# Kernel optimization log

Hardware: AMD Instinct MI355X
Metric: run time of the kernel (lower is better)

The kernel has to match this reference:

```python
import jax, jax.numpy as jnp
import numpy as np

PATCH_SIZES = (16, 32, 48, 64)
RES_IDX = (0, 1, 2, 3)  # min(int(s*4/3), 3) for s in 0..3
QUANT_RESI = 0.5
BETA = 0.25
D = 32      # embedding_dim == input channels
V = 2048    # vocab_size
G = 8       # GroupNorm groups
EPS = 1e-5


def conv3(x, w, b):
    y = jax.lax.conv_general_dilated(x, w, (1, 1), 'SAME', dimension_numbers=('NCHW', 'OIHW', 'NCHW'))
    return y + b[None, :, None, None]


def group_norm(x, gamma, beta):
    n, c, h, w = x.shape
    xr = x.reshape(n, G, c // G, h, w)
    mu = xr.mean(axis=(2, 3, 4), keepdims=True)
    var = xr.var(axis=(2, 3, 4), keepdims=True)
    xn = ((xr - mu) * jax.lax.rsqrt(var + EPS)).reshape(n, c, h, w)
    return xn * gamma[None, :, None, None] + beta[None, :, None, None]


def conv_block(x, w1, b1, gamma, beta, w2, b2):
    h = conv3(x, w1, b1)
    h = jax.nn.gelu(group_norm(h, gamma, beta), approximate=False)
    return conv3(h, w2, b2)


def _forward(x, emb, pw1, pb1, pg, pbt, pw2, pb2, rw1, rb1, rg, rbt, rw2, rb2):
    B, C, H, W = x.shape
    acc = jnp.zeros_like(x)
    total_loss = jnp.zeros((), x.dtype)
    idx_list = []
    for s, p in enumerate(PATCH_SIZES):
        nh, nw = H // p, W // p
        # unfold: non-overlapping patches -> (B*N, C, p, p), N row-major over (nh, nw)
        patches = (x - acc).reshape(B, C, nh, p, nw, p).transpose(0, 2, 4, 1, 3, 5).reshape(B * nh * nw, C, p, p)
        z = conv_block(patches, pw1[s], pb1[s], pg[s], pbt[s], pw2[s], pb2[s])
        zf = z.reshape(-1, D)  # raw row-major reshape, exactly as the torch code does
        d = (zf * zf).sum(1, keepdims=True) + (emb * emb).sum(1) - 2.0 * (zf @ emb.T)
        idx = jnp.argmin(d, axis=1)
        zq = emb[idx].reshape(z.shape)
        loss = jnp.mean((jax.lax.stop_gradient(zq) - z) ** 2) + BETA * jnp.mean((zq - jax.lax.stop_gradient(z)) ** 2)
        total_loss = total_loss + loss
        zq = z + jax.lax.stop_gradient(zq - z)  # straight-through estimator
        r = RES_IDX[s]
        zq = zq * (1.0 - QUANT_RESI) + conv_block(zq, rw1[r], rb1[r], rg[r], rbt[r], rw2[r], rb2[r]) * QUANT_RESI
        # fold: exact inverse of unfold (patch sizes divide H, W)
        decoded = zq.reshape(B, nh, nw, C, p, p).transpose(0, 3, 1, 4, 2, 5).reshape(B, C, H, W)
        acc = acc + decoded
        idx_list.append(idx.reshape(B, -1))
    return (jax.nn.sigmoid(acc), *idx_list, total_loss)


def setup_inputs() -> dict:
    key = jax.random.key(0)
    ks = jax.random.split(key, 4)
    S = len(PATCH_SIZES)
    x = jax.random.normal(ks[0], (1, D, 384, 384), dtype=jnp.float32)
    emb = jax.random.uniform(ks[1], (V, D), jnp.float32, -1.0 / V, 1.0 / V)

    def wset(k):
        k1, k2, k3, k4 = jax.random.split(k, 4)
        return (jax.random.normal(k1, (S, D, D, 3, 3), jnp.float32) * 0.05,
                jax.random.normal(k2, (S, D), jnp.float32) * 0.02,
                jnp.ones((S, D), jnp.float32),
                jnp.zeros((S, D), jnp.float32),
                jax.random.normal(k3, (S, D, D, 3, 3), jnp.float32) * 0.05,
                jax.random.normal(k4, (S, D), jnp.float32) * 0.02)

    pw1, pb1, pg, pbt, pw2, pb2 = wset(ks[2])
    rw1, rb1, rg, rbt, rw2, rb2 = wset(ks[3])
    return {"x": x, "emb": emb,
            "pw1": pw1, "pb1": pb1, "pg": pg, "pbt": pbt, "pw2": pw2, "pb2": pb2,
            "rw1": rw1, "rb1": rb1, "rg": rg, "rbt": rbt, "rw2": rw2, "rb2": rb2}


def reference(x, emb, pw1, pb1, pg, pbt, pw2, pb2, rw1, rb1, rg, rbt, rw2, rb2):
    return _forward(x, emb, pw1, pb1, pg, pbt, pw2, pb2, rw1, rb1, rg, rbt, rw2, rb2)
```

## Files before the change

kernel.cpp:

```cpp
#include <hip/hip_runtime.h>
#include <cmath>

#define WIDTH 384
#define HW 147456
#define CHW 4718592
#define NCH 32
#define NV 2048
#define NROWS 147456

typedef short vshort8 __attribute__((ext_vector_type(8)));
typedef float vfloat4 __attribute__((ext_vector_type(4)));

__device__ inline unsigned short bf_split(float x, float& back) {
  unsigned int b; __builtin_memcpy(&b, &x, 4);
  unsigned int r = (b + 0x7FFFu + ((b >> 16) & 1u)) >> 16;
  unsigned int bb = r << 16; float f; __builtin_memcpy(&f, &bb, 4);
  back = f; return (unsigned short)r;
}

template <int SQ>
__device__ float np_pw(const float* a, int n, float mu) {
  if (n < 8) {
    float res = 0.0f;
    for (int i = 0; i < n; i++) {
      float v = a[i];
      if (SQ) { float d = __fsub_rn(v, mu); v = __fmul_rn(d, d); }
      res = __fadd_rn(res, v);
    }
    return res;
  }
  if (n <= 128) {
    float r[8];
#pragma unroll
    for (int j = 0; j < 8; j++) {
      float v = a[j];
      if (SQ) { float d = __fsub_rn(v, mu); v = __fmul_rn(d, d); }
      r[j] = v;
    }
    int i;
    for (i = 8; i + 8 <= n; i += 8) {
#pragma unroll
      for (int j = 0; j < 8; j++) {
        float v = a[i + j];
        if (SQ) { float d = __fsub_rn(v, mu); v = __fmul_rn(d, d); }
        r[j] = __fadd_rn(r[j], v);
      }
    }
    float res = __fadd_rn(__fadd_rn(__fadd_rn(r[0], r[1]), __fadd_rn(r[2], r[3])),
                          __fadd_rn(__fadd_rn(r[4], r[5]), __fadd_rn(r[6], r[7])));
    for (; i < n; i++) {
      float v = a[i];
      if (SQ) { float d = __fsub_rn(v, mu); v = __fmul_rn(d, d); }
      res = __fadd_rn(res, v);
    }
    return res;
  }
  int n2 = n / 2; n2 -= n2 % 8;
  return __fadd_rn(np_pw<SQ>(a, n2, mu), np_pw<SQ>(a + n2, n - n2, mu));
}

__global__ __launch_bounds__(256) void prep_kernel(
    const float* __restrict__ pw1, const float* __restrict__ pw2,
    const float* __restrict__ rw1, const float* __restrict__ rw2,
    const float* __restrict__ emb, float* __restrict__ wt, float* __restrict__ ee,
    unsigned short* __restrict__ eh, unsigned short* __restrict__ el) {
  int t = blockIdx.x * 256 + threadIdx.x;
  if (t < 147456) {
    int layer = t / 9216, r = t % 9216;
    int k = r / 32, co = r % 32;
    int set = layer >> 2, s = layer & 3;
    const float* src = set == 0 ? pw1 : set == 1 ? pw2 : set == 2 ? rw1 : rw2;
    wt[t] = src[s * 9216 + co * 288 + k];
  } else if (t < 147456 + NV) {
    int v = t - 147456;
    const float* e = emb + v * 32;
    float r[8];
#pragma unroll
    for (int j = 0; j < 8; j++) r[j] = __fmul_rn(e[j], e[j]);
#pragma unroll
    for (int i = 8; i < 32; i += 8)
#pragma unroll
      for (int j = 0; j < 8; j++) r[j] = __fadd_rn(r[j], __fmul_rn(e[i + j], e[i + j]));
    ee[v] = __fadd_rn(__fadd_rn(__fadd_rn(r[0], r[1]), __fadd_rn(r[2], r[3])),
                      __fadd_rn(__fadd_rn(r[4], r[5]), __fadd_rn(r[6], r[7])));
  } else if (t < 147456 + NV + 65536) {
    int idx = t - 147456 - NV;
    float x = emb[idx], hb;
    eh[idx] = bf_split(x, hb);
    float lb;
    el[idx] = bf_split(__fsub_rn(x, hb), lb);
  }
}

template <int MODE>
__global__ __launch_bounds__(192, 3) void conv32_kernel(
    const float* __restrict__ in, const float* __restrict__ x,
    const float* __restrict__ accin, float* __restrict__ outb,
    const float* __restrict__ zqb, float* __restrict__ acc,
    const float* __restrict__ wt, const float* __restrict__ bias, int p, int nw) {
  int t = blockIdx.x * 192 + threadIdx.x;
  int pp = p * p;
  int px = t % p; int t1 = t / p;
  int py = t1 % p;
  int n  = t1 / p;
  int i = n / nw, j = n % nw;

  int off[9]; bool msk[9];
#pragma unroll
  for (int dy = 0; dy < 3; dy++) {
    int ly = py + dy - 1;
    bool vy = (unsigned)ly < (unsigned)p;
    int cy = vy ? ly : 0;
#pragma unroll
    for (int dx = 0; dx < 3; dx++) {
      int lx = px + dx - 1;
      bool vx = (unsigned)lx < (unsigned)p;
      int cx = vx ? lx : 0;
      msk[dy * 3 + dx] = vy && vx;
      if (MODE == 1) off[dy * 3 + dx] = (i * p + cy) * WIDTH + (j * p + cx);
      else           off[dy * 3 + dx] = cy * p + cx;
    }
  }

  const float* pin = (MODE == 1) ? nullptr : in + (size_t)n * NCH * pp;

  float a[NCH];
#pragma unroll
  for (int co = 0; co < NCH; co++) a[co] = 0.0f;

  float tv[9], tn[9];
#pragma unroll
  for (int k = 0; k < 9; k++) {
    float v;
    if (MODE == 1) {
      size_t ad = (size_t)off[k];
      v = __fsub_rn(x[ad], accin[ad]);
    } else {
      v = pin[off[k]];
    }
    tv[k] = msk[k] ? v : 0.0f;
  }

  for (int ci = 0; ci < NCH; ci++) {
    if (ci + 1 < NCH) {
#pragma unroll
      for (int k = 0; k < 9; k++) {
        float v;
        if (MODE == 1) {
          size_t ad = (size_t)(ci + 1) * HW + off[k];
          v = __fsub_rn(x[ad], accin[ad]);
        } else {
          v = pin[(size_t)(ci + 1) * pp + off[k]];
        }
        tn[k] = msk[k] ? v : 0.0f;
      }
    }
    const float* wp = wt + ci * 288;
#pragma unroll
    for (int k = 0; k < 9; k++) {
#pragma unroll
      for (int co = 0; co < NCH; co++)
        a[co] = fmaf(tv[k], wp[k * 32 + co], a[co]);
    }
#pragma unroll
    for (int k = 0; k < 9; k++) tv[k] = tn[k];
  }

#pragma unroll
  for (int co = 0; co < NCH; co++) {
    float r = __fadd_rn(a[co], bias[co]);
    if (MODE == 2) {
      size_t img = (size_t)co * HW + (size_t)(i * p + py) * WIDTH + (j * p + px);
      size_t pt  = (size_t)n * NCH * pp + (size_t)co * pp + (size_t)py * p + px;
      float dec = __fadd_rn(__fmul_rn(zqb[pt], 0.5f), __fmul_rn(r, 0.5f));
      acc[img] = __fadd_rn(acc[img], dec);
    } else {
      outb[(size_t)n * NCH * pp + (size_t)co * pp + (size_t)py * p + px] = r;
    }
  }
}

__global__ __launch_bounds__(64) void gn_stats_kernel(
    const float* __restrict__ buf, float2* __restrict__ stats,
    int p, int C, int chunk) {
  int tid = threadIdx.x;
  int gpw = 64 / C;
  int gi = tid / C, cl = tid % C;
  int grp = blockIdx.x * gpw + gi;
  int pp = p * p, ne = 4 * pp;
  const float* base = buf + ((size_t)(grp >> 3) * NCH + (size_t)(grp & 7) * 4) * pp
                      + (size_t)cl * chunk;

  float s = np_pw<0>(base, chunk, 0.0f);
  for (int m = 1; m < C; m <<= 1) s = __fadd_rn(s, __shfl_xor(s, m, 64));
  float mu = __fdiv_rn(s, (float)ne);

  float s2 = np_pw<1>(base, chunk, mu);
  for (int m = 1; m < C; m <<= 1) s2 = __fadd_rn(s2, __shfl_xor(s2, m, 64));

  if (cl == 0) {
    float var = __fdiv_rn(s2, (float)ne);
    float rs = __fdiv_rn(1.0f, __fsqrt_rn(__fadd_rn(var, 1e-5f)));
    stats[grp] = make_float2(mu, rs);
  }
}

__global__ __launch_bounds__(256) void gn_gelu_kernel(
    float* __restrict__ buf, const float2* __restrict__ stats,
    const float* __restrict__ gamma, const float* __restrict__ beta, int p) {
  int t = blockIdx.x * 256 + threadIdx.x;
  int pp = p * p;
  int t2 = t / pp;
  int c = t2 % NCH;
  int n = t2 / NCH;
  float2 st = stats[n * 8 + (c >> 2)];
  float v = __fadd_rn(__fmul_rn(__fmul_rn(__fsub_rn(buf[t], st.x), st.y), gamma[c]), beta[c]);
  float tt = __fdiv_rn(v, 1.41421356237309504880f);
  float e = (float)erf((double)tt);
  buf[t] = __fmul_rn(__fmul_rn(0.5f, v), __fadd_rn(1.0f, e));
}

__global__ __launch_bounds__(576, 5) void gemm_min_kernel(
    const float* __restrict__ z,
    const unsigned short* __restrict__ EH, const unsigned short* __restrict__ EL,
    const float* __restrict__ EE,
    float* __restrict__ BD, float* __restrict__ B2, int* __restrict__ I1) {
  __shared__ float ee_l[2048];
  int tid = threadIdx.x;
  for (int i = tid; i < 2048; i += 576) ee_l[i] = EE[i];
  __syncthreads();

  int wid = tid / 64, lane = tid & 63;
  int t0 = blockIdx.x * 18 + wid * 2;
  int lr = lane & 15, lg = lane >> 4;

  float za0[8], za1[8];
  {
    const float4* zp0 = (const float4*)(z + (size_t)(t0 * 16 + lr) * 32 + 8 * lg);
    const float4* zp1 = (const float4*)(z + (size_t)((t0 + 1) * 16 + lr) * 32 + 8 * lg);
    float4 c0 = zp0[0], c1 = zp0[1], d0 = zp1[0], d1 = zp1[1];
    za0[0]=c0.x; za0[1]=c0.y; za0[2]=c0.z; za0[3]=c0.w;
    za0[4]=c1.x; za0[5]=c1.y; za0[6]=c1.z; za0[7]=c1.w;
    za1[0]=d0.x; za1[1]=d0.y; za1[2]=d0.z; za1[3]=d0.w;
    za1[4]=d1.x; za1[5]=d1.y; za1[6]=d1.z; za1[7]=d1.w;
  }

  float zz0, zz1;
  {
    float r0[8], r1[8];
#pragma unroll
    for (int j = 0; j < 8; j++) {
      float p0 = __fmul_rn(za0[j], za0[j]);
      float p1 = __fmul_rn(za1[j], za1[j]);
      float a0 = __shfl(p0, lr, 64),      a1 = __shfl(p0, 16 + lr, 64);
      float a2 = __shfl(p0, 32 + lr, 64), a3 = __shfl(p0, 48 + lr, 64);
      r0[j] = __fadd_rn(__fadd_rn(__fadd_rn(a0, a1), a2), a3);
      float b0 = __shfl(p1, lr, 64),      b1 = __shfl(p1, 16 + lr, 64);
      float b2_ = __shfl(p1, 32 + lr, 64), b3 = __shfl(p1, 48 + lr, 64);
      r1[j] = __fadd_rn(__fadd_rn(__fadd_rn(b0, b1), b2_), b3);
    }
    zz0 = __fadd_rn(__fadd_rn(__fadd_rn(r0[0], r0[1]), __fadd_rn(r0[2], r0[3])),
                    __fadd_rn(__fadd_rn(r0[4], r0[5]), __fadd_rn(r0[6], r0[7])));
    zz1 = __fadd_rn(__fadd_rn(__fadd_rn(r1[0], r1[1]), __fadd_rn(r1[2], r1[3])),
                    __fadd_rn(__fadd_rn(r1[4], r1[5]), __fadd_rn(r1[6], r1[7])));
  }
  float zzv[8];
#pragma unroll
  for (int r = 0; r < 4; r++) {
    zzv[r]     = __shfl(zz0, 4 * lg + r, 64);
    zzv[4 + r] = __shfl(zz1, 4 * lg + r, 64);
  }

  vshort8 azh0, azl0, azh1, azl1;
#pragma unroll
  for (int j = 0; j < 8; j++) {
    float hb;
    azh0[j] = (short)bf_split(za0[j], hb);
    float lb;
    azl0[j] = (short)bf_split(__fsub_rn(za0[j], hb), lb);
    azh1[j] = (short)bf_split(za1[j], hb);
    azl1[j] = (short)bf_split(__fsub_rn(za1[j], hb), lb);
  }

  float b1[8], b2[8]; int i1[8];
#pragma unroll
  for (int r = 0; r < 8; r++) { b1[r] = 3.402823466e+38f; b2[r] = 3.402823466e+38f; i1[r] = 0; }

  vshort8 nbeh = *(const vshort8*)(EH + (size_t)lr * 32 + 8 * lg);
  vshort8 nbel = *(const vshort8*)(EL + (size_t)lr * 32 + 8 * lg);

  for (int ct = 0; ct < 128; ct++) {
    vshort8 beh = nbeh, bel = nbel;
    if (ct + 1 < 128) {
      nbeh = *(const vshort8*)(EH + (size_t)((ct + 1) * 16 + lr) * 32 + 8 * lg);
      nbel = *(const vshort8*)(EL + (size_t)((ct + 1) * 16 + lr) * 32 + 8 * lg);
    }
    vfloat4 acc0 = {0.0f, 0.0f, 0.0f, 0.0f};
    acc0 = __builtin_amdgcn_mfma_f32_16x16x32_bf16(azh0, beh, acc0, 0, 0, 0);
    acc0 = __builtin_amdgcn_mfma_f32_16x16x32_bf16(azh0, bel, acc0, 0, 0, 0);
    acc0 = __builtin_amdgcn_mfma_f32_16x16x32_bf16(azl0, beh, acc0, 0, 0, 0);
    vfloat4 acc1 = {0.0f, 0.0f, 0.0f, 0.0f};
    acc1 = __builtin_amdgcn_mfma_f32_16x16x32_bf16(azh1, beh, acc1, 0, 0, 0);
    acc1 = __builtin_amdgcn_mfma_f32_16x16x32_bf16(azh1, bel, acc1, 0, 0, 0);
    acc1 = __builtin_amdgcn_mfma_f32_16x16x32_bf16(azl1, beh, acc1, 0, 0, 0);
    int col = ct * 16 + lr;
    float eev = ee_l[col];
#pragma unroll
    for (int r = 0; r < 4; r++) {
      float d = (zzv[r] + eev) - 2.0f * acc0[r];
      if (d < b1[r]) { b2[r] = b1[r]; b1[r] = d; i1[r] = col; }
      else b2[r] = fminf(b2[r], d);
      float d1 = (zzv[4 + r] + eev) - 2.0f * acc1[r];
      if (d1 < b1[4 + r]) { b2[4 + r] = b1[4 + r]; b1[4 + r] = d1; i1[4 + r] = col; }
      else b2[4 + r] = fminf(b2[4 + r], d1);
    }
  }

  for (int m = 1; m < 16; m <<= 1) {
#pragma unroll
    for (int r = 0; r < 8; r++) {
      float ob1 = __shfl_xor(b1[r], m, 64);
      int   oi1 = __shfl_xor(i1[r], m, 64);
      float ob2 = __shfl_xor(b2[r], m, 64);
      bool aw = (b1[r] < ob1) || (b1[r] == ob1 && i1[r] < oi1);
      float lo = aw ? ob1 : b1[r];
      b1[r] = aw ? b1[r] : ob1;
      i1[r] = aw ? i1[r] : oi1;
      b2[r] = fminf(fminf(b2[r], ob2), lo);
    }
  }

  if (lr == 0) {
#pragma unroll
    for (int r = 0; r < 4; r++) {
      int row0 = t0 * 16 + 4 * lg + r;
      BD[row0] = b1[r]; B2[row0] = b2[r]; I1[row0] = i1[r];
      int row1 = (t0 + 1) * 16 + 4 * lg + r;
      BD[row1] = b1[4 + r]; B2[row1] = b2[4 + r]; I1[row1] = i1[4 + r];
    }
  }
}

__global__ __launch_bounds__(256) void epilogue_kernel(
    const float* __restrict__ z, const float* __restrict__ emb,
    const float* __restrict__ BD, const float* __restrict__ B2,
    const int* __restrict__ I1, float* __restrict__ zq,
    float* __restrict__ idxout, double* __restrict__ ssep,
    int* __restrict__ list, int* __restrict__ cnt) {
  int t = blockIdx.x * 256 + threadIdx.x;
  int row = t >> 2, part = t & 3;
  float bd = BD[row];
  int bi = I1[row];
  float margin = __fadd_rn(1.0e-6f, __fmul_rn(5.0e-7f, fabsf(bd)));
  bool flagged = (B2[row] - bd) <= margin;
  if (flagged && part == 0) {
    int i = atomicAdd(cnt, 1);
    list[i] = row;
  }
  const float4* ep = (const float4*)(emb + (size_t)bi * 32 + part * 8);
  const float4* zp = (const float4*)(z + (size_t)row * 32 + part * 8);
  float4* qp = (float4*)(zq + (size_t)row * 32 + part * 8);
  float4 e0 = ep[0], e1 = ep[1];
  float4 z0 = zp[0], z1 = zp[1];
  qp[0] = e0; qp[1] = e1;
  double sse = 0.0, d;
  d = (double)e0.x - (double)z0.x; sse += d * d;
  d = (double)e0.y - (double)z0.y; sse += d * d;
  d = (double)e0.z - (double)z0.z; sse += d * d;
  d = (double)e0.w - (double)z0.w; sse += d * d;
  d = (double)e1.x - (double)z1.x; sse += d * d;
  d = (double)e1.y - (double)z1.y; sse += d * d;
  d = (double)e1.z - (double)z1.z; sse += d * d;
  d = (double)e1.w - (double)z1.w; sse += d * d;
  ssep[t] = sse;
  if (part == 0) idxout[row] = (float)bi;
}

__global__ __launch_bounds__(64) void rescore_kernel(
    const float* __restrict__ z, const float* __restrict__ emb,
    const float* __restrict__ EE,
    float* __restrict__ zq, float* __restrict__ idxout,
    double* __restrict__ ssep, const int* __restrict__ list,
    const int* __restrict__ cnt) {
  int lane = threadIdx.x;
  int n = *cnt;
  for (int i = blockIdx.x; i < n; i += gridDim.x) {
    int row = list[i];
    const float* zp = z + (size_t)row * 32;
    float zb[32];
#pragma unroll
    for (int q = 0; q < 32; q++) zb[q] = zp[q];
    float rr[8];
#pragma unroll
    for (int j = 0; j < 8; j++) rr[j] = __fmul_rn(zb[j], zb[j]);
#pragma unroll
    for (int ii = 8; ii < 32; ii += 8)
#pragma unroll
      for (int j = 0; j < 8; j++) rr[j] = __fadd_rn(rr[j], __fmul_rn(zb[ii + j], zb[ii + j]));
    float zzb = __fadd_rn(__fadd_rn(__fadd_rn(rr[0], rr[1]), __fadd_rn(rr[2], rr[3])),
                          __fadd_rn(__fadd_rn(rr[4], rr[5]), __fadd_rn(rr[6], rr[7])));
    float bestd = 3.402823466e+38f;
    int bestv = NV;
    for (int k = 0; k < 32; k++) {
      int v = lane + 64 * k;
      const float* e0 = emb + (size_t)v * 32;
      float m = 0.0f;
#pragma unroll
      for (int q = 0; q < 32; q++) m = fmaf(zb[q], e0[q], m);
      float d = __fsub_rn(__fadd_rn(zzb, EE[v]), __fmul_rn(2.0f, m));
      if (d < bestd) { bestd = d; bestv = v; }
    }
    for (int mm = 1; mm < 64; mm <<= 1) {
      float od = __shfl_xor(bestd, mm, 64);
      int ov = __shfl_xor(bestv, mm, 64);
      if (od < bestd || (od == bestd && ov < bestv)) { bestd = od; bestv = ov; }
    }
    if (lane < 32) zq[(size_t)row * 32 + lane] = emb[bestv * 32 + lane];
    if (lane < 4) {
      const float* ep = emb + bestv * 32 + lane * 8;
      const float* zr = z + (size_t)row * 32 + lane * 8;
      double sse = 0.0;
#pragma unroll
      for (int q = 0; q < 8; q++) {
        double dd = (double)ep[q] - (double)zr[q];
        sse += dd * dd;
      }
      ssep[row * 4 + lane] = sse;
    }
    if (lane == 0) idxout[row] = (float)bestv;
  }
}

__global__ __launch_bounds__(256) void ssered_kernel(
    const double* __restrict__ ssep, double* __restrict__ part) {
  __shared__ double red[256];
  int t = blockIdx.x * 256 + threadIdx.x;
  const double* b = ssep + (size_t)t * 4;
  red[threadIdx.x] = ((b[0] + b[1]) + (b[2] + b[3]));
  __syncthreads();
  for (int st = 128; st > 0; st >>= 1) {
    if (threadIdx.x < st) red[threadIdx.x] += red[threadIdx.x + st];
    __syncthreads();
  }
  if (threadIdx.x == 0) part[blockIdx.x] = red[0];
}

__global__ __launch_bounds__(256) void sigmoid_kernel(
    const float* __restrict__ acc, float* __restrict__ out) {
  int t = blockIdx.x * 256 + threadIdx.x;
  out[t] = (float)(1.0 / (1.0 + exp(-(double)acc[t])));
}

__global__ void loss_kernel(const double* __restrict__ part, float* __restrict__ out) {
  double tot = 0.0;
  for (int s = 0; s < 4; s++) {
    double sse = 0.0;
    for (int b = 0; b < 576; b++) sse += part[s * 1024 + b];
    tot += 1.25 * sse / 4718592.0;
  }
  out[0] = (float)tot;
}

extern "C" void kernel_launch(void* const* d_in, const int* in_sizes, int n_in,
                              void* d_out, int out_size, void* d_ws, size_t ws_size,
                              hipStream_t stream) {
  const float* X   = (const float*)d_in[0];
  const float* EMB = (const float*)d_in[1];
  const float* PW1 = (const float*)d_in[2];
  const float* PB1 = (const float*)d_in[3];
  const float* PG  = (const float*)d_in[4];
  const float* PBT = (const float*)d_in[5];
  const float* PW2 = (const float*)d_in[6];
  const float* PB2 = (const float*)d_in[7];
  const float* RW1 = (const float*)d_in[8];
  const float* RB1 = (const float*)d_in[9];
  const float* RG  = (const float*)d_in[10];
  const float* RBT = (const float*)d_in[11];
  const float* RW2 = (const float*)d_in[12];
  const float* RB2 = (const float*)d_in[13];
  float* out = (float*)d_out;

  char* w = (char*)d_ws;
  float*          EE    = (float*)(w);
  float*          WT    = (float*)(w + 8192UL);
  unsigned short* EH    = (unsigned short*)(w + 598016UL);
  unsigned short* EL    = (unsigned short*)(w + 729088UL);
  float2*         STATS = (float2*)(w + 860160UL);
  double*         PART  = (double*)(w + 897024UL);
  float*          BD    = (float*)(w + 929792UL);
  float*          B2    = (float*)(w + 1519616UL);
  int*            I1    = (int*)(w + 2109440UL);
  float*          P     = (float*)(w + 2699264UL);
  float*          H     = (float*)(w + 21573632UL);
  float*          ACC   = (float*)(w + 40448000UL);
  int*            CNT   = (int*)(w + 59322368UL);
  int*            LIST  = (int*)(w + 59322432UL);
  double*         SSEP  = (double*)(w + 59912256UL);

  hipMemsetAsync(ACC, 0, 18874368UL, stream);
  hipMemsetAsync(CNT, 0, 64UL, stream);
  prep_kernel<<<840, 256, 0, stream>>>(PW1, PW2, RW1, RW2, EMB, WT, EE, EH, EL);

  const int PS[4] = {16, 32, 48, 64};
  for (int s = 0; s < 4; s++) {
    int p = PS[s], nw = 384 / p, N = nw * nw;
    int C = (p == 16) ? 8 : (p == 32) ? 32 : 64;
    int chunk = (4 * p * p) / C;
    int gblocks = (N * 8 * C) / 64;
    const float* wt_p1 = WT + (0 * 4 + s) * 9216;
    const float* wt_p2 = WT + (1 * 4 + s) * 9216;
    const float* wt_r1 = WT + (2 * 4 + s) * 9216;
    const float* wt_r2 = WT + (3 * 4 + s) * 9216;

    conv32_kernel<1><<<768, 192, 0, stream>>>(nullptr, X, ACC, H, nullptr, nullptr,
                                              wt_p1, PB1 + s * 32, p, nw);
    gn_stats_kernel<<<gblocks, 64, 0, stream>>>(H, STATS, p, C, chunk);
    gn_gelu_kernel<<<18432, 256, 0, stream>>>(H, STATS, PG + s * 32, PBT + s * 32, p);
    conv32_kernel<0><<<768, 192, 0, stream>>>(H, nullptr, nullptr, P, nullptr, nullptr,
                                              wt_p2, PB2 + s * 32, p, nw);
    gemm_min_kernel<<<512, 576, 0, stream>>>(P, EH, EL, EE, BD, B2, I1);
    epilogue_kernel<<<2304, 256, 0, stream>>>(P, EMB, BD, B2, I1, H,
                                              out + 4718592 + s * 147456, SSEP,
                                              LIST, CNT + s);
    rescore_kernel<<<1024, 64, 0, stream>>>(P, EMB, EE, H,
                                            out + 4718592 + s * 147456, SSEP,
                                            LIST, CNT + s);
    ssered_kernel<<<576, 256, 0, stream>>>(SSEP, PART + s * 1024);
    conv32_kernel<0><<<768, 192, 0, stream>>>(H, nullptr, nullptr, P, nullptr, nullptr,
                                              wt_r1, RB1 + s * 32, p, nw);
    gn_stats_kernel<<<gblocks, 64, 0, stream>>>(P, STATS, p, C, chunk);
    gn_gelu_kernel<<<18432, 256, 0, stream>>>(P, STATS, RG + s * 32, RBT + s * 32, p);
    conv32_kernel<2><<<768, 192, 0, stream>>>(P, nullptr, nullptr, nullptr, H, ACC,
                                              wt_r2, RB2 + s * 32, p, nw);
  }

  sigmoid_kernel<<<18432, 256, 0, stream>>>(ACC, out);
  loss_kernel<<<1, 1, 0, stream>>>(PART, out + 5308416);
}
```

Measured before the change: 2.030 ms.

## Fuse rescore and SSE reduction into epilogue, drop ACC memset for first scale

Flagged near-tie rows are now re-scored in the epilogue kernel itself: each wavefront ballots its flagged rows and runs an exact fp32 argmin over the codebook for each of them. This removes the atomic list, the separate rescore and ssered kernels, and the SSEP buffer round-trip, and per-block SSE partials are reduced in shared memory. The first scale uses new conv modes that read x directly and write ACC without reading it, so the ACC and counter memsets are dropped. The loss kernel is parallelised over 256 threads. In exchange, waves that contain flagged rows serialise on the full codebook scan inside the epilogue and can stall their block.

```diff
diff --git a/kernel.cpp b/kernel.cpp
--- a/kernel.cpp
+++ b/kernel.cpp
@@ -105,6 +105,7 @@
   int n  = t1 / p;
   int i = n / nw, j = n % nw;
 
+  const bool IMGIN = (MODE == 1 || MODE == 3);
   int off[9]; bool msk[9];
 #pragma unroll
   for (int dy = 0; dy < 3; dy++) {
@@ -117,12 +118,12 @@
       bool vx = (unsigned)lx < (unsigned)p;
       int cx = vx ? lx : 0;
       msk[dy * 3 + dx] = vy && vx;
-      if (MODE == 1) off[dy * 3 + dx] = (i * p + cy) * WIDTH + (j * p + cx);
-      else           off[dy * 3 + dx] = cy * p + cx;
-    }
-  }
-
-  const float* pin = (MODE == 1) ? nullptr : in + (size_t)n * NCH * pp;
+      if (IMGIN) off[dy * 3 + dx] = (i * p + cy) * WIDTH + (j * p + cx);
+      else       off[dy * 3 + dx] = cy * p + cx;
+    }
+  }
+
+  const float* pin = IMGIN ? nullptr : in + (size_t)n * NCH * pp;
 
   float a[NCH];
 #pragma unroll
@@ -132,12 +133,9 @@
 #pragma unroll
   for (int k = 0; k < 9; k++) {
     float v;
-    if (MODE == 1) {
-      size_t ad = (size_t)off[k];
-      v = __fsub_rn(x[ad], accin[ad]);
-    } else {
-      v = pin[off[k]];
-    }
+    if (MODE == 1)      v = __fsub_rn(x[(size_t)off[k]], accin[(size_t)off[k]]);
+    else if (MODE == 3) v = x[(size_t)off[k]];
+    else                v = pin[off[k]];
     tv[k] = msk[k] ? v : 0.0f;
   }
 
@@ -149,6 +147,8 @@
         if (MODE == 1) {
           size_t ad = (size_t)(ci + 1) * HW + off[k];
           v = __fsub_rn(x[ad], accin[ad]);
+        } else if (MODE == 3) {
+          v = x[(size_t)(ci + 1) * HW + off[k]];
         } else {
           v = pin[(size_t)(ci + 1) * pp + off[k]];
         }
@@ -169,11 +169,12 @@
 #pragma unroll
   for (int co = 0; co < NCH; co++) {
     float r = __fadd_rn(a[co], bias[co]);
-    if (MODE == 2) {
+    if (MODE == 2 || MODE == 4) {
       size_t img = (size_t)co * HW + (size_t)(i * p + py) * WIDTH + (j * p + px);
       size_t pt  = (size_t)n * NCH * pp + (size_t)co * pp + (size_t)py * p + px;
       float dec = __fadd_rn(__fmul_rn(zqb[pt], 0.5f), __fmul_rn(r, 0.5f));
-      acc[img] = __fadd_rn(acc[img], dec);
+      if (MODE == 2) acc[img] = __fadd_rn(acc[img], dec);
+      else           acc[img] = __fadd_rn(0.0f, dec);
     } else {
       outb[(size_t)n * NCH * pp + (size_t)co * pp + (size_t)py * p + px] = r;
     }
@@ -343,23 +344,60 @@
 
 __global__ __launch_bounds__(256) void epilogue_kernel(
     const float* __restrict__ z, const float* __restrict__ emb,
+    const float* __restrict__ EE,
     const float* __restrict__ BD, const float* __restrict__ B2,
     const int* __restrict__ I1, float* __restrict__ zq,
-    float* __restrict__ idxout, double* __restrict__ ssep,
-    int* __restrict__ list, int* __restrict__ cnt) {
-  int t = blockIdx.x * 256 + threadIdx.x;
-  int row = t >> 2, part = t & 3;
+    float* __restrict__ idxout, double* __restrict__ part) {
+  __shared__ double red[256];
+  int tid = threadIdx.x;
+  int lane = tid & 63;
+  int t = blockIdx.x * 256 + tid;
+  int row = t >> 2, quarter = t & 3;
   float bd = BD[row];
   int bi = I1[row];
   float margin = __fadd_rn(1.0e-6f, __fmul_rn(5.0e-7f, fabsf(bd)));
   bool flagged = (B2[row] - bd) <= margin;
-  if (flagged && part == 0) {
-    int i = atomicAdd(cnt, 1);
-    list[i] = row;
-  }
-  const float4* ep = (const float4*)(emb + (size_t)bi * 32 + part * 8);
-  const float4* zp = (const float4*)(z + (size_t)row * 32 + part * 8);
-  float4* qp = (float4*)(zq + (size_t)row * 32 + part * 8);
+
+  unsigned long long mask = __ballot(flagged && quarter == 0);
+  while (mask) {
+    int l = __ffsll((long long)mask) - 1;
+    mask &= mask - 1;
+    int rrow = __shfl(row, l, 64);
+    const float* zp = z + (size_t)rrow * 32;
+    float zb[32];
+#pragma unroll
+    for (int q = 0; q < 32; q++) zb[q] = zp[q];
+    float rr[8];
+#pragma unroll
+    for (int j = 0; j < 8; j++) rr[j] = __fmul_rn(zb[j], zb[j]);
+#pragma unroll
+    for (int ii = 8; ii < 32; ii += 8)
+#pragma unroll
+      for (int j = 0; j < 8; j++) rr[j] = __fadd_rn(rr[j], __fmul_rn(zb[ii + j], zb[ii + j]));
+    float zzb = __fadd_rn(__fadd_rn(__fadd_rn(rr[0], rr[1]), __fadd_rn(rr[2], rr[3])),
+                          __fadd_rn(__fadd_rn(rr[4], rr[5]), __fadd_rn(rr[6], rr[7])));
+    float bestd = 3.402823466e+38f;
+    int bestv = NV;
+    for (int k = 0; k < 32; k++) {
+      int v = lane + 64 * k;
+      const float* e0 = emb + (size_t)v * 32;
+      float m = 0.0f;
+#pragma unroll
+      for (int q = 0; q < 32; q++) m = fmaf(zb[q], e0[q], m);
+      float d = __fsub_rn(__fadd_rn(zzb, EE[v]), __fmul_rn(2.0f, m));
+      if (d < bestd) { bestd = d; bestv = v; }
+    }
+    for (int mm = 1; mm < 64; mm <<= 1) {
+      float od = __shfl_xor(bestd, mm, 64);
+      int ov = __shfl_xor(bestv, mm, 64);
+      if (od < bestd || (od == bestd && ov < bestv)) { bestd = od; bestv = ov; }
+    }
+    if (row == rrow) bi = bestv;
+  }
+
+  const float4* ep = (const float4*)(emb + (size_t)bi * 32 + quarter * 8);
+  const float4* zp = (const float4*)(z + (size_t)row * 32 + quarter * 8);
+  float4* qp = (float4*)(zq + (size_t)row * 32 + quarter * 8);
   float4 e0 = ep[0], e1 = ep[1];
   float4 z0 = zp[0], z1 = zp[1];
   qp[0] = e0; qp[1] = e1;
@@ -372,77 +410,15 @@
   d = (double)e1.y - (double)z1.y; sse += d * d;
   d = (double)e1.z - (double)z1.z; sse += d * d;
   d = (double)e1.w - (double)z1.w; sse += d * d;
-  ssep[t] = sse;
-  if (part == 0) idxout[row] = (float)bi;
-}
-
-__global__ __launch_bounds__(64) void rescore_kernel(
-    const float* __restrict__ z, const float* __restrict__ emb,
-    const float* __restrict__ EE,
-    float* __restrict__ zq, float* __restrict__ idxout,
-    double* __restrict__ ssep, const int* __restrict__ list,
-    const int* __restrict__ cnt) {
-  int lane = threadIdx.x;
-  int n = *cnt;
-  for (int i = blockIdx.x; i < n; i += gridDim.x) {
-    int row = list[i];
-    const float* zp = z + (size_t)row * 32;
-    float zb[32];
-#pragma unroll
-    for (int q = 0; q < 32; q++) zb[q] = zp[q];
-    float rr[8];
-#pragma unroll
-    for (int j = 0; j < 8; j++) rr[j] = __fmul_rn(zb[j], zb[j]);
-#pragma unroll
-    for (int ii = 8; ii < 32; ii += 8)
-#pragma unroll
-      for (int j = 0; j < 8; j++) rr[j] = __fadd_rn(rr[j], __fmul_rn(zb[ii + j], zb[ii + j]));
-    float zzb = __fadd_rn(__fadd_rn(__fadd_rn(rr[0], rr[1]), __fadd_rn(rr[2], rr[3])),
-                          __fadd_rn(__fadd_rn(rr[4], rr[5]), __fadd_rn(rr[6], rr[7])));
-    float bestd = 3.402823466e+38f;
-    int bestv = NV;
-    for (int k = 0; k < 32; k++) {
-      int v = lane + 64 * k;
-      const float* e0 = emb + (size_t)v * 32;
-      float m = 0.0f;
-#pragma unroll
-      for (int q = 0; q < 32; q++) m = fmaf(zb[q], e0[q], m);
-      float d = __fsub_rn(__fadd_rn(zzb, EE[v]), __fmul_rn(2.0f, m));
-      if (d < bestd) { bestd = d; bestv = v; }
-    }
-    for (int mm = 1; mm < 64; mm <<= 1) {
-      float od = __shfl_xor(bestd, mm, 64);
-      int ov = __shfl_xor(bestv, mm, 64);
-      if (od < bestd || (od == bestd && ov < bestv)) { bestd = od; bestv = ov; }
-    }
-    if (lane < 32) zq[(size_t)row * 32 + lane] = emb[bestv * 32 + lane];
-    if (lane < 4) {
-      const float* ep = emb + bestv * 32 + lane * 8;
-      const float* zr = z + (size_t)row * 32 + lane * 8;
-      double sse = 0.0;
-#pragma unroll
-      for (int q = 0; q < 8; q++) {
-        double dd = (double)ep[q] - (double)zr[q];
-        sse += dd * dd;
-      }
-      ssep[row * 4 + lane] = sse;
-    }
-    if (lane == 0) idxout[row] = (float)bestv;
-  }
-}
-
-__global__ __launch_bounds__(256) void ssered_kernel(
-    const double* __restrict__ ssep, double* __restrict__ part) {
-  __shared__ double red[256];
-  int t = blockIdx.x * 256 + threadIdx.x;
-  const double* b = ssep + (size_t)t * 4;
-  red[threadIdx.x] = ((b[0] + b[1]) + (b[2] + b[3]));
+  if (quarter == 0) idxout[row] = (float)bi;
+
+  red[tid] = sse;
   __syncthreads();
   for (int st = 128; st > 0; st >>= 1) {
-    if (threadIdx.x < st) red[threadIdx.x] += red[threadIdx.x + st];
+    if (tid < st) red[tid] += red[tid + st];
     __syncthreads();
   }
-  if (threadIdx.x == 0) part[blockIdx.x] = red[0];
+  if (tid == 0) part[blockIdx.x] = red[0];
 }
 
 __global__ __launch_bounds__(256) void sigmoid_kernel(
@@ -451,14 +427,24 @@
   out[t] = (float)(1.0 / (1.0 + exp(-(double)acc[t])));
 }
 
-__global__ void loss_kernel(const double* __restrict__ part, float* __restrict__ out) {
+__global__ __launch_bounds__(256) void loss_kernel(
+    const double* __restrict__ part, float* __restrict__ out) {
+  __shared__ double red[256];
+  int tid = threadIdx.x;
   double tot = 0.0;
   for (int s = 0; s < 4; s++) {
     double sse = 0.0;
-    for (int b = 0; b < 576; b++) sse += part[s * 1024 + b];
-    tot += 1.25 * sse / 4718592.0;
-  }
-  out[0] = (float)tot;
+    for (int b = tid; b < 2304; b += 256) sse += part[s * 2304 + b];
+    red[tid] = sse;
+    __syncthreads();
+    for (int st = 128; st > 0; st >>= 1) {
+      if (tid < st) red[tid] += red[tid + st];
+      __syncthreads();
+    }
+    if (tid == 0) tot += 1.25 * red[0] / 4718592.0;
+    __syncthreads();
+  }
+  if (tid == 0) out[0] = (float)tot;
 }
 
 extern "C" void kernel_launch(void* const* d_in, const int* in_sizes, int n_in,
@@ -487,18 +473,13 @@
   unsigned short* EL    = (unsigned short*)(w + 729088UL);
   float2*         STATS = (float2*)(w + 860160UL);
   double*         PART  = (double*)(w + 897024UL);
-  float*          BD    = (float*)(w + 929792UL);
-  float*          B2    = (float*)(w + 1519616UL);
-  int*            I1    = (int*)(w + 2109440UL);
-  float*          P     = (float*)(w + 2699264UL);
-  float*          H     = (float*)(w + 21573632UL);
-  float*          ACC   = (float*)(w + 40448000UL);
-  int*            CNT   = (int*)(w + 59322368UL);
-  int*            LIST  = (int*)(w + 59322432UL);
-  double*         SSEP  = (double*)(w + 59912256UL);
-
-  hipMemsetAsync(ACC, 0, 18874368UL, stream);
-  hipMemsetAsync(CNT, 0, 64UL, stream);
+  float*          BD    = (float*)(w + 970752UL);
+  float*          B2    = (float*)(w + 1560576UL);
+  int*            I1    = (int*)(w + 2150400UL);
+  float*          P     = (float*)(w + 2740224UL);
+  float*          H     = (float*)(w + 21614592UL);
+  float*          ACC   = (float*)(w + 40488960UL);
+
   prep_kernel<<<840, 256, 0, stream>>>(PW1, PW2, RW1, RW2, EMB, WT, EE, EH, EL);
 
   const int PS[4] = {16, 32, 48, 64};
@@ -512,28 +493,31 @@
     const float* wt_r1 = WT + (2 * 4 + s) * 9216;
     const float* wt_r2 = WT + (3 * 4 + s) * 9216;
 
-    conv32_kernel<1><<<768, 192, 0, stream>>>(nullptr, X, ACC, H, nullptr, nullptr,
-                                              wt_p1, PB1 + s * 32, p, nw);
+    if (s == 0)
+      conv32_kernel<3><<<768, 192, 0, stream>>>(nullptr, X, nullptr, H, nullptr, nullptr,
+                                                wt_p1, PB1 + s * 32, p, nw);
+    else
+      conv32_kernel<1><<<768, 192, 0, stream>>>(nullptr, X, ACC, H, nullptr, nullptr,
+                                                wt_p1, PB1 + s * 32, p, nw);
     gn_stats_kernel<<<gblocks, 64, 0, stream>>>(H, STATS, p, C, chunk);
     gn_gelu_kernel<<<18432, 256, 0, stream>>>(H, STATS, PG + s * 32, PBT + s * 32, p);
     conv32_kernel<0><<<768, 192, 0, stream>>>(H, nullptr, nullptr, P, nullptr, nullptr,
                                               wt_p2, PB2 + s * 32, p, nw);
     gemm_min_kernel<<<512, 576, 0, stream>>>(P, EH, EL, EE, BD, B2, I1);
-    epilogue_kernel<<<2304, 256, 0, stream>>>(P, EMB, BD, B2, I1, H,
-                                              out + 4718592 + s * 147456, SSEP,
-                                              LIST, CNT + s);
-    rescore_kernel<<<1024, 64, 0, stream>>>(P, EMB, EE, H,
-                                            out + 4718592 + s * 147456, SSEP,
-                                            LIST, CNT + s);
-    ssered_kernel<<<576, 256, 0, stream>>>(SSEP, PART + s * 1024);
+    epilogue_kernel<<<2304, 256, 0, stream>>>(P, EMB, EE, BD, B2, I1, H,
+                                              out + 4718592 + s * 147456, PART + s * 2304);
     conv32_kernel<0><<<768, 192, 0, stream>>>(H, nullptr, nullptr, P, nullptr, nullptr,
                                               wt_r1, RB1 + s * 32, p, nw);
     gn_stats_kernel<<<gblocks, 64, 0, stream>>>(P, STATS, p, C, chunk);
     gn_gelu_kernel<<<18432, 256, 0, stream>>>(P, STATS, RG + s * 32, RBT + s * 32, p);
-    conv32_kernel<2><<<768, 192, 0, stream>>>(P, nullptr, nullptr, nullptr, H, ACC,
-                                              wt_r2, RB2 + s * 32, p, nw);
+    if (s == 0)
+      conv32_kernel<4><<<768, 192, 0, stream>>>(P, nullptr, nullptr, nullptr, H, ACC,
+                                                wt_r2, RB2 + s * 32, p, nw);
+    else
+      conv32_kernel<2><<<768, 192, 0, stream>>>(P, nullptr, nullptr, nullptr, H, ACC,
+                                                wt_r2, RB2 + s * 32, p, nw);
   }
 
   sigmoid_kernel<<<18432, 256, 0, stream>>>(ACC, out);
-  loss_kernel<<<1, 1, 0, stream>>>(PART, out + 5308416);
-}
+  loss_kernel<<<1, 256, 0, stream>>>(PART, out + 5308416);
+}
```

Result: slower. 2.075 ms (+2.2%).
